# Kernel tuning notes

Hardware: AMD Instinct MI355X
Metric: run time of the kernel (lower is better)

The kernel has to match this reference:

```python
import jax, jax.numpy as jnp
import numpy as np

COMMITMENT_COST = 0.25
EMBEDDING_DIM = 64
NUM_EMBEDDINGS = 512
BATCH, SEQ = 64, 4096


def setup_inputs() -> dict:
    key = jax.random.key(0)
    k1, k2, k3 = jax.random.split(key, 3)
    return {
        "inputs": jax.random.normal(k1, (BATCH, SEQ, EMBEDDING_DIM), dtype=jnp.float32),
        "embedding": jax.random.normal(k2, (NUM_EMBEDDINGS, EMBEDDING_DIM), dtype=jnp.float32),
        "ema_cluster_size": jax.random.uniform(k3, (NUM_EMBEDDINGS,), dtype=jnp.float32),
    }


def reference(inputs, embedding, ema_cluster_size):
    # inputs: [B, T, D]; embedding: [K, D]; ema_cluster_size: [K]
    input_shape = inputs.shape
    flat = inputs.reshape(-1, EMBEDDING_DIM)  # [N, D]
    distances = (
        jnp.sum(flat * flat, axis=1, keepdims=True)
        + jnp.sum(embedding * embedding, axis=1)[None, :]
        - 2.0 * (flat @ embedding.T)
    )
    # cluster-size weighting (as in the source module)
    distances = distances * jnp.sqrt(ema_cluster_size)[None, :]
    encoding_indices = jnp.argmin(distances, axis=1)  # [N]
    # one-hot @ codebook == gather
    quantized = embedding[encoding_indices].reshape(input_shape)
    e_latent_loss = jnp.mean((jax.lax.stop_gradient(quantized) - inputs) ** 2)
    loss = COMMITMENT_COST * e_latent_loss
    # straight-through estimator
    quantized_st = inputs + jax.lax.stop_gradient(quantized - inputs)
    return quantized_st, loss, encoding_indices[:, None]
```

## Files before the change

### kernel.cpp

```cpp
#include <hip/hip_runtime.h>
#include <math.h>

#define D 64
#define K 512

typedef __attribute__((ext_vector_type(8))) short short8;
typedef __attribute__((ext_vector_type(4))) float f32x4;

#define WS_E2    256
#define WS_SQ    2304
#define WS_ETS   4352
#define WS_BP    8448
#define WS_WL    139520
#define WS_PART  1188096
#define WS_PART2 1204480

#define KEYMASK 0xFFFFFE00u
#define DIST_BIAS 0.0625f

__device__ __forceinline__ unsigned short f32_to_bf16_rne(float f)
{
    unsigned int u = __float_as_uint(f);
    unsigned int r = (u + 0x7FFFu + ((u >> 16) & 1u)) >> 16;
    return (unsigned short)r;
}
__device__ __forceinline__ float bf16_to_f32(unsigned short h)
{
    return __uint_as_float(((unsigned int)h) << 16);
}

__device__ __forceinline__ float np_sumsq64(const float* v)
{
#pragma clang fp contract(off)
    float p[64];
#pragma unroll
    for (int i = 0; i < 64; ++i) p[i] = v[i] * v[i];
    float r[8];
#pragma unroll
    for (int j = 0; j < 8; ++j) r[j] = p[j];
#pragma unroll
    for (int b = 8; b < 64; b += 8) {
#pragma unroll
        for (int j = 0; j < 8; ++j) r[j] += p[b + j];
    }
    return ((r[0] + r[1]) + (r[2] + r[3])) + ((r[4] + r[5]) + (r[6] + r[7]));
}

__global__ __launch_bounds__(256) void vq_pack_prep(
    const float* __restrict__ emb,
    const float* __restrict__ cs,
    unsigned short* __restrict__ Bp,
    float* __restrict__ e2,
    float* __restrict__ sq,
    float2* __restrict__ ets,
    int* __restrict__ cnt)
{
    int i = blockIdx.x * blockDim.x + threadIdx.x;
    if (i < 65536) {
        int j    = i & 7;
        int lane = (i >> 3) & 63;
        int frag = (i >> 9) & 3;
        int t    = (i >> 11) & 31;
        int kc   = frag & 1;
        int sB   = frag >> 1;
        int code = t * 16 + (lane & 15);
        int d    = kc * 32 + (lane >> 4) * 8 + j;
        float v = emb[code * 64 + d];
        unsigned short b0 = f32_to_bf16_rne(v);
        Bp[i] = (sB == 0) ? b0 : f32_to_bf16_rne(v - bf16_to_f32(b0));
    } else if (i < 66048) {
        int k = i - 65536;
        float er[64];
        const float* ek = emb + (size_t)k * D;
#pragma unroll
        for (int d = 0; d < 64; ++d) er[d] = ek[d];
        float e2v = np_sumsq64(er);
        float sqv = (float)sqrt((double)cs[k]);
        e2[k] = e2v;
        sq[k] = sqv;
        ets[k] = make_float2(e2v * sqv + DIST_BIAS, 2.0f * sqv);
    } else if (i == 66048) {
        *cnt = 0;
    }
}

__global__ __launch_bounds__(512) void vq_screen(
    const float* __restrict__ x,
    const float* __restrict__ emb,
    const float2* __restrict__ ets,
    const unsigned short* __restrict__ Bp,
    float* __restrict__ out_q,
    float* __restrict__ out_idx,
    int* __restrict__ wl,
    int* __restrict__ cnt,
    double* __restrict__ partial)
{
    __shared__ unsigned short BpS[65536];
    __shared__ double ls[8];

    const int wave = threadIdx.x >> 6;
    const int lane = threadIdx.x & 63;
    const int quad = lane >> 4;
    const int n16  = lane & 15;

    {
        const float4* src = (const float4*)Bp;
        float4* dst = (float4*)BpS;
#pragma unroll
        for (int it = 0; it < 16; ++it)
            dst[threadIdx.x + it * 512] = src[threadIdx.x + it * 512];
    }
    __syncthreads();

    double s = 0.0;

    for (int pass = 0; pass < 2; ++pass) {
        const int n0 = blockIdx.x * 1024 + pass * 512 + wave * 64;

        short8 A0[4][2], A1[4][2];
        f32x4 negx2h[4];
#pragma unroll
        for (int rt = 0; rt < 4; ++rt) {
            float sx = 0.0f;
#pragma unroll
            for (int kc = 0; kc < 2; ++kc) {
                const float* src = x + (size_t)(n0 + rt * 16 + n16) * 64
                                   + kc * 32 + quad * 8;
                float4 v0 = *(const float4*)(src);
                float4 v1 = *(const float4*)(src + 4);
                float xv[8] = {v0.x, v0.y, v0.z, v0.w, v1.x, v1.y, v1.z, v1.w};
#pragma unroll
                for (int j = 0; j < 8; ++j) {
                    float v = xv[j];
                    unsigned short b0 = f32_to_bf16_rne(v);
                    unsigned short b1 = f32_to_bf16_rne(v - bf16_to_f32(b0));
                    A0[rt][kc][j] = (short)b0;
                    A1[rt][kc][j] = (short)b1;
                    sx = fmaf(v, v, sx);
                }
            }
            sx += __shfl_xor(sx, 16, 64);
            sx += __shfl_xor(sx, 32, 64);
#pragma unroll
            for (int r = 0; r < 4; ++r)
                negx2h[rt][r] = -0.5f * __shfl(sx, quad * 4 + r, 64);
        }

        unsigned k1[4][4], k2[4][4];
#pragma unroll
        for (int rt = 0; rt < 4; ++rt)
#pragma unroll
            for (int r = 0; r < 4; ++r) { k1[rt][r] = 0xFFFFFFFFu; k2[rt][r] = 0xFFFFFFFFu; }

#pragma unroll 2
        for (int t = 0; t < 32; ++t) {
            const unsigned short* bp = BpS + t * 2048 + lane * 8;
            const short8 B00 = *(const short8*)(bp);
            const short8 B01 = *(const short8*)(bp + 512);
            const short8 B10 = *(const short8*)(bp + 1024);
            const short8 B11 = *(const short8*)(bp + 1536);
            float2 et = ets[t * 16 + n16];
            unsigned cbits = (unsigned)(t * 16 + n16);

#pragma unroll
            for (int rt = 0; rt < 4; ++rt) {
                f32x4 acc = negx2h[rt];
                acc = __builtin_amdgcn_mfma_f32_16x16x32_bf16(A0[rt][0], B00, acc, 0, 0, 0);
                acc = __builtin_amdgcn_mfma_f32_16x16x32_bf16(A0[rt][1], B01, acc, 0, 0, 0);
                acc = __builtin_amdgcn_mfma_f32_16x16x32_bf16(A0[rt][0], B10, acc, 0, 0, 0);
                acc = __builtin_amdgcn_mfma_f32_16x16x32_bf16(A0[rt][1], B11, acc, 0, 0, 0);
                acc = __builtin_amdgcn_mfma_f32_16x16x32_bf16(A1[rt][0], B00, acc, 0, 0, 0);
                acc = __builtin_amdgcn_mfma_f32_16x16x32_bf16(A1[rt][1], B01, acc, 0, 0, 0);

#pragma unroll
                for (int r = 0; r < 4; ++r) {
                    float dist = fmaf(-et.y, acc[r], et.x);
                    unsigned key = (__float_as_uint(dist) & KEYMASK) | cbits;
                    unsigned a1 = k1[rt][r];
                    unsigned a2;
                    asm("v_med3_u32 %0, %1, %2, %3"
                        : "=v"(a2) : "v"(a1), "v"(k2[rt][r]), "v"(key));
                    k2[rt][r] = a2;
                    k1[rt][r] = a1 < key ? a1 : key;
                }
            }
        }

#pragma unroll
        for (int rt = 0; rt < 4; ++rt)
#pragma unroll
            for (int r = 0; r < 4; ++r) {
                unsigned a1 = k1[rt][r], a2 = k2[rt][r];
#pragma unroll
                for (int w = 1; w < 16; w <<= 1) {
                    unsigned o1 = (unsigned)__shfl_xor((int)a1, w, 64);
                    unsigned o2 = (unsigned)__shfl_xor((int)a2, w, 64);
                    unsigned mx  = a1 > o1 ? a1 : o1;
                    a1 = a1 < o1 ? a1 : o1;
                    unsigned mn2 = a2 < o2 ? a2 : o2;
                    a2 = mn2 < mx ? mn2 : mx;
                }
                k1[rt][r] = a1; k2[rt][r] = a2;
            }

        unsigned pk[4][4];
#pragma unroll
        for (int rt = 0; rt < 4; ++rt)
#pragma unroll
            for (int r = 0; r < 4; ++r) {
                float d1f = __uint_as_float(k1[rt][r] & KEYMASK);
                float d2f = __uint_as_float(k2[rt][r] & KEYMASK);
                int   i1  = (int)(k1[rt][r] & 0x1FFu);
                int   flg = (d2f - d1f) <= (0.01f + 2.0e-4f * d2f);
                pk[rt][r] = (unsigned)i1 | (flg ? 0x8000u : 0u);
                if (n16 == 0) {
                    int p = n0 + rt * 16 + quad * 4 + r;
                    out_idx[p] = (float)i1;
                    if (flg) { int slot = atomicAdd(cnt, 1); wl[slot] = p; }
                }
            }

        int src = (n16 >> 2) * 16 + n16;
#pragma unroll
        for (int rt = 0; rt < 4; ++rt) {
            unsigned p0 = (unsigned)__shfl((int)pk[rt][0], src, 64);
            unsigned p1 = (unsigned)__shfl((int)pk[rt][1], src, 64);
            unsigned p2 = (unsigned)__shfl((int)pk[rt][2], src, 64);
            unsigned p3 = (unsigned)__shfl((int)pk[rt][3], src, 64);
            int rr = n16 & 3;
            unsigned pm = (rr == 0) ? p0 : (rr == 1) ? p1 : (rr == 2) ? p2 : p3;
            int bim = (int)(pm & 0x1FFu);
            int flg = (int)((pm >> 15) & 1u);
            if (!flg) {
                int prow = n0 + rt * 16 + n16;
#pragma unroll
                for (int kc = 0; kc < 2; ++kc) {
                    const float* xs = x   + (size_t)prow * 64 + kc * 32 + quad * 8;
                    const float* es = emb + (size_t)bim  * 64 + kc * 32 + quad * 8;
                    float4 xv0 = *(const float4*)(xs);
                    float4 xv1 = *(const float4*)(xs + 4);
                    float4 ev0 = *(const float4*)(es);
                    float4 ev1 = *(const float4*)(es + 4);
                    float4 o0, o1;
                    float t0, t1, t2, t3, t4, t5, t6, t7;
                    {
#pragma clang fp contract(off)
                        t0 = ev0.x - xv0.x; o0.x = xv0.x + t0;
                        t1 = ev0.y - xv0.y; o0.y = xv0.y + t1;
                        t2 = ev0.z - xv0.z; o0.z = xv0.z + t2;
                        t3 = ev0.w - xv0.w; o0.w = xv0.w + t3;
                        t4 = ev1.x - xv1.x; o1.x = xv1.x + t4;
                        t5 = ev1.y - xv1.y; o1.y = xv1.y + t5;
                        t6 = ev1.z - xv1.z; o1.z = xv1.z + t6;
                        t7 = ev1.w - xv1.w; o1.w = xv1.w + t7;
                    }
                    float* od = out_q + (size_t)prow * 64 + kc * 32 + quad * 8;
                    *(float4*)(od)     = o0;
                    *(float4*)(od + 4) = o1;
                    s += (double)t0 * t0 + (double)t1 * t1
                       + (double)t2 * t2 + (double)t3 * t3
                       + (double)t4 * t4 + (double)t5 * t5
                       + (double)t6 * t6 + (double)t7 * t7;
                }
            }
        }
    }

#pragma unroll
    for (int off = 32; off > 0; off >>= 1)
        s += __shfl_down(s, off, 64);
    if (lane == 0) ls[wave] = s;
    __syncthreads();
    if (threadIdx.x == 0)
        partial[blockIdx.x] = ls[0] + ls[1] + ls[2] + ls[3]
                            + ls[4] + ls[5] + ls[6] + ls[7];
}

__global__ __launch_bounds__(256) void vq_exact(
    const float* __restrict__ x,
    const float* __restrict__ emb,
    const float* __restrict__ e2,
    const float* __restrict__ sq,
    const int* __restrict__ wl,
    const int* __restrict__ cnt,
    float* __restrict__ out_idx,
    float* __restrict__ out_q,
    double* __restrict__ partial2)
{
    const int lane = threadIdx.x & 63;
    const int gw   = blockIdx.x * 4 + (threadIdx.x >> 6);
    const int nw   = gridDim.x * 4;
    const int cv   = *cnt;

    for (int w = gw; w < cv; w += nw) {
        int p = wl[w];
        const float* xrow = x + (size_t)p * 64;
        float row[64];
#pragma unroll
        for (int i = 0; i < 16; ++i) {
            float4 v = ((const float4*)xrow)[i];
            row[4 * i + 0] = v.x; row[4 * i + 1] = v.y;
            row[4 * i + 2] = v.z; row[4 * i + 3] = v.w;
        }
        float x2 = np_sumsq64(row);

        float bd = INFINITY;
        int   bc = 0;
        for (int t = 0; t < 8; ++t) {
            int c = t * 64 + lane;
            const float* er = emb + (size_t)c * 64;
            float acc = 0.0f;
#pragma unroll
            for (int d = 0; d < 64; ++d)
                acc = fmaf(row[d], er[d], acc);
            float dist;
            {
#pragma clang fp contract(off)
                dist = ((x2 + e2[c]) - 2.0f * acc) * sq[c];
            }
            if (dist < bd) { bd = dist; bc = c; }
        }
#pragma unroll
        for (int wd = 1; wd < 64; wd <<= 1) {
            float od = __shfl_xor(bd, wd, 64);
            int   oc = __shfl_xor(bc, wd, 64);
            if (od < bd || (od == bd && oc < bc)) { bd = od; bc = oc; }
        }
        if (lane == 0) out_idx[p] = (float)bc;

        float xv = x[(size_t)p * 64 + lane];
        float qv = emb[(size_t)bc * 64 + lane];
        float t, o;
        {
#pragma clang fp contract(off)
            t = qv - xv;
            o = xv + t;
        }
        out_q[(size_t)p * 64 + lane] = o;
        double dd = (double)t * (double)t;
#pragma unroll
        for (int off = 32; off > 0; off >>= 1)
            dd += __shfl_down(dd, off, 64);
        if (lane == 0) partial2[w] = dd;
    }
}

__global__ __launch_bounds__(256) void vq_finalize(
    const double* __restrict__ partial,
    const double* __restrict__ partial2,
    const int* __restrict__ cnt,
    float* __restrict__ loss_out,
    int nblk, double inv_count)
{
    double s = 0.0;
    for (int i = threadIdx.x; i < nblk; i += 256) s += partial[i];
    int cv = *cnt;
    for (int w = threadIdx.x; w < cv; w += 256) s += partial2[w];
#pragma unroll
    for (int off = 32; off > 0; off >>= 1)
        s += __shfl_down(s, off, 64);
    __shared__ double ls[4];
    if ((threadIdx.x & 63) == 0) ls[threadIdx.x >> 6] = s;
    __syncthreads();
    if (threadIdx.x == 0) {
        double total = ls[0] + ls[1] + ls[2] + ls[3];
        loss_out[0] = (float)(0.25 * total * inv_count);
    }
}

extern "C" void kernel_launch(void* const* d_in, const int* in_sizes, int n_in,
                              void* d_out, int out_size, void* d_ws, size_t ws_size,
                              hipStream_t stream)
{
    const float* x   = (const float*)d_in[0];
    const float* emb = (const float*)d_in[1];
    const float* cs  = (const float*)d_in[2];

    const int N = in_sizes[0] / D;

    float* out      = (float*)d_out;
    float* out_q    = out;
    float* out_loss = out + (size_t)N * D;
    float* out_idx  = out_loss + 1;

    char* ws = (char*)d_ws;
    int*            cnt      = (int*)ws;
    float*          e2       = (float*)(ws + WS_E2);
    float*          sq       = (float*)(ws + WS_SQ);
    float2*         ets      = (float2*)(ws + WS_ETS);
    unsigned short* Bp       = (unsigned short*)(ws + WS_BP);
    int*            wl       = (int*)(ws + WS_WL);
    double*         partial  = (double*)(ws + WS_PART);
    double*         partial2 = (double*)(ws + WS_PART2);

    const int nblk_screen = N / 1024;

    vq_pack_prep<<<259, 256, 0, stream>>>(emb, cs, Bp, e2, sq, ets, cnt);
    vq_screen<<<nblk_screen, 512, 0, stream>>>(x, emb, ets, Bp,
                                               out_q, out_idx, wl, cnt, partial);
    vq_exact<<<512, 256, 0, stream>>>(x, emb, e2, sq, wl, cnt,
                                      out_idx, out_q, partial2);
    vq_finalize<<<1, 256, 0, stream>>>(partial, partial2, cnt, out_loss,
                                       nblk_screen, 1.0 / ((double)N * (double)D));
}
```

Measured before the change: 204.3 us.

## Halve screen LDS footprint by staging codebook in two halves, one pass per block

The screening kernel now keeps only half of the packed bf16 codebook in shared memory (64KB instead of 128KB). It runs the first 256 codes, then reloads the second half between barriers. It also caches the ets table in LDS, and each block handles 512 rows in a single pass instead of 1024 rows in two, so twice as many blocks launch. The smaller LDS footprint is meant to let two blocks share a CU and to spread work over more blocks, at the cost of loading the codebook twice per block with an extra barrier in the middle.

```diff
diff --git a/kernel.cpp b/kernel.cpp
--- a/kernel.cpp
+++ b/kernel.cpp
@@ -95,173 +95,216 @@
     int* __restrict__ cnt,
     double* __restrict__ partial)
 {
-    __shared__ unsigned short BpS[65536];
+    __shared__ unsigned short BpS[32768];
+    __shared__ float2 etsS[512];
     __shared__ double ls[8];
 
     const int wave = threadIdx.x >> 6;
     const int lane = threadIdx.x & 63;
     const int quad = lane >> 4;
     const int n16  = lane & 15;
+    const int n0   = blockIdx.x * 512 + wave * 64;
 
     {
         const float4* src = (const float4*)Bp;
         float4* dst = (float4*)BpS;
 #pragma unroll
-        for (int it = 0; it < 16; ++it)
+        for (int it = 0; it < 8; ++it)
             dst[threadIdx.x + it * 512] = src[threadIdx.x + it * 512];
+        etsS[threadIdx.x] = ets[threadIdx.x];
     }
     __syncthreads();
 
     double s = 0.0;
 
-    for (int pass = 0; pass < 2; ++pass) {
-        const int n0 = blockIdx.x * 1024 + pass * 512 + wave * 64;
-
-        short8 A0[4][2], A1[4][2];
-        f32x4 negx2h[4];
+    short8 A0[4][2], A1[4][2];
+    f32x4 negx2h[4];
+#pragma unroll
+    for (int rt = 0; rt < 4; ++rt) {
+        float sx = 0.0f;
+#pragma unroll
+        for (int kc = 0; kc < 2; ++kc) {
+            const float* src = x + (size_t)(n0 + rt * 16 + n16) * 64
+                               + kc * 32 + quad * 8;
+            float4 v0 = *(const float4*)(src);
+            float4 v1 = *(const float4*)(src + 4);
+            float xv[8] = {v0.x, v0.y, v0.z, v0.w, v1.x, v1.y, v1.z, v1.w};
+#pragma unroll
+            for (int j = 0; j < 8; ++j) {
+                float v = xv[j];
+                unsigned short b0 = f32_to_bf16_rne(v);
+                unsigned short b1 = f32_to_bf16_rne(v - bf16_to_f32(b0));
+                A0[rt][kc][j] = (short)b0;
+                A1[rt][kc][j] = (short)b1;
+                sx = fmaf(v, v, sx);
+            }
+        }
+        sx += __shfl_xor(sx, 16, 64);
+        sx += __shfl_xor(sx, 32, 64);
+#pragma unroll
+        for (int r = 0; r < 4; ++r)
+            negx2h[rt][r] = -0.5f * __shfl(sx, quad * 4 + r, 64);
+    }
+
+    unsigned k1[4][4], k2[4][4];
+#pragma unroll
+    for (int rt = 0; rt < 4; ++rt)
+#pragma unroll
+        for (int r = 0; r < 4; ++r) { k1[rt][r] = 0xFFFFFFFFu; k2[rt][r] = 0xFFFFFFFFu; }
+
+#pragma unroll 2
+    for (int t = 0; t < 16; ++t) {
+        const unsigned short* bp = BpS + t * 2048 + lane * 8;
+        const short8 B00 = *(const short8*)(bp);
+        const short8 B01 = *(const short8*)(bp + 512);
+        const short8 B10 = *(const short8*)(bp + 1024);
+        const short8 B11 = *(const short8*)(bp + 1536);
+        float2 et = etsS[t * 16 + n16];
+        unsigned cbits = (unsigned)(t * 16 + n16);
+
 #pragma unroll
         for (int rt = 0; rt < 4; ++rt) {
-            float sx = 0.0f;
+            f32x4 acc = negx2h[rt];
+            acc = __builtin_amdgcn_mfma_f32_16x16x32_bf16(A0[rt][0], B00, acc, 0, 0, 0);
+            acc = __builtin_amdgcn_mfma_f32_16x16x32_bf16(A0[rt][1], B01, acc, 0, 0, 0);
+            acc = __builtin_amdgcn_mfma_f32_16x16x32_bf16(A0[rt][0], B10, acc, 0, 0, 0);
+            acc = __builtin_amdgcn_mfma_f32_16x16x32_bf16(A0[rt][1], B11, acc, 0, 0, 0);
+            acc = __builtin_amdgcn_mfma_f32_16x16x32_bf16(A1[rt][0], B00, acc, 0, 0, 0);
+            acc = __builtin_amdgcn_mfma_f32_16x16x32_bf16(A1[rt][1], B01, acc, 0, 0, 0);
+
+#pragma unroll
+            for (int r = 0; r < 4; ++r) {
+                float dist = fmaf(-et.y, acc[r], et.x);
+                unsigned key = (__float_as_uint(dist) & KEYMASK) | cbits;
+                unsigned a1 = k1[rt][r];
+                unsigned a2;
+                asm("v_med3_u32 %0, %1, %2, %3"
+                    : "=v"(a2) : "v"(a1), "v"(k2[rt][r]), "v"(key));
+                k2[rt][r] = a2;
+                k1[rt][r] = a1 < key ? a1 : key;
+            }
+        }
+    }
+
+    __syncthreads();
+    {
+        const float4* src = (const float4*)(Bp + 32768);
+        float4* dst = (float4*)BpS;
+#pragma unroll
+        for (int it = 0; it < 8; ++it)
+            dst[threadIdx.x + it * 512] = src[threadIdx.x + it * 512];
+    }
+    __syncthreads();
+
+#pragma unroll 2
+    for (int t = 16; t < 32; ++t) {
+        const unsigned short* bp = BpS + (t - 16) * 2048 + lane * 8;
+        const short8 B00 = *(const short8*)(bp);
+        const short8 B01 = *(const short8*)(bp + 512);
+        const short8 B10 = *(const short8*)(bp + 1024);
+        const short8 B11 = *(const short8*)(bp + 1536);
+        float2 et = etsS[t * 16 + n16];
+        unsigned cbits = (unsigned)(t * 16 + n16);
+
+#pragma unroll
+        for (int rt = 0; rt < 4; ++rt) {
+            f32x4 acc = negx2h[rt];
+            acc = __builtin_amdgcn_mfma_f32_16x16x32_bf16(A0[rt][0], B00, acc, 0, 0, 0);
+            acc = __builtin_amdgcn_mfma_f32_16x16x32_bf16(A0[rt][1], B01, acc, 0, 0, 0);
+            acc = __builtin_amdgcn_mfma_f32_16x16x32_bf16(A0[rt][0], B10, acc, 0, 0, 0);
+            acc = __builtin_amdgcn_mfma_f32_16x16x32_bf16(A0[rt][1], B11, acc, 0, 0, 0);
+            acc = __builtin_amdgcn_mfma_f32_16x16x32_bf16(A1[rt][0], B00, acc, 0, 0, 0);
+            acc = __builtin_amdgcn_mfma_f32_16x16x32_bf16(A1[rt][1], B01, acc, 0, 0, 0);
+
+#pragma unroll
+            for (int r = 0; r < 4; ++r) {
+                float dist = fmaf(-et.y, acc[r], et.x);
+                unsigned key = (__float_as_uint(dist) & KEYMASK) | cbits;
+                unsigned a1 = k1[rt][r];
+                unsigned a2;
+                asm("v_med3_u32 %0, %1, %2, %3"
+                    : "=v"(a2) : "v"(a1), "v"(k2[rt][r]), "v"(key));
+                k2[rt][r] = a2;
+                k1[rt][r] = a1 < key ? a1 : key;
+            }
+        }
+    }
+
+#pragma unroll
+    for (int rt = 0; rt < 4; ++rt)
+#pragma unroll
+        for (int r = 0; r < 4; ++r) {
+            unsigned a1 = k1[rt][r], a2 = k2[rt][r];
+#pragma unroll
+            for (int w = 1; w < 16; w <<= 1) {
+                unsigned o1 = (unsigned)__shfl_xor((int)a1, w, 64);
+                unsigned o2 = (unsigned)__shfl_xor((int)a2, w, 64);
+                unsigned mx  = a1 > o1 ? a1 : o1;
+                a1 = a1 < o1 ? a1 : o1;
+                unsigned mn2 = a2 < o2 ? a2 : o2;
+                a2 = mn2 < mx ? mn2 : mx;
+            }
+            k1[rt][r] = a1; k2[rt][r] = a2;
+        }
+
+    unsigned pk[4][4];
+#pragma unroll
+    for (int rt = 0; rt < 4; ++rt)
+#pragma unroll
+        for (int r = 0; r < 4; ++r) {
+            float d1f = __uint_as_float(k1[rt][r] & KEYMASK);
+            float d2f = __uint_as_float(k2[rt][r] & KEYMASK);
+            int   i1  = (int)(k1[rt][r] & 0x1FFu);
+            int   flg = (d2f - d1f) <= (0.01f + 2.0e-4f * d2f);
+            pk[rt][r] = (unsigned)i1 | (flg ? 0x8000u : 0u);
+            if (n16 == 0) {
+                int p = n0 + rt * 16 + quad * 4 + r;
+                out_idx[p] = (float)i1;
+                if (flg) { int slot = atomicAdd(cnt, 1); wl[slot] = p; }
+            }
+        }
+
+    int src = (n16 >> 2) * 16 + n16;
+#pragma unroll
+    for (int rt = 0; rt < 4; ++rt) {
+        unsigned p0 = (unsigned)__shfl((int)pk[rt][0], src, 64);
+        unsigned p1 = (unsigned)__shfl((int)pk[rt][1], src, 64);
+        unsigned p2 = (unsigned)__shfl((int)pk[rt][2], src, 64);
+        unsigned p3 = (unsigned)__shfl((int)pk[rt][3], src, 64);
+        int rr = n16 & 3;
+        unsigned pm = (rr == 0) ? p0 : (rr == 1) ? p1 : (rr == 2) ? p2 : p3;
+        int bim = (int)(pm & 0x1FFu);
+        int flg = (int)((pm >> 15) & 1u);
+        if (!flg) {
+            int prow = n0 + rt * 16 + n16;
 #pragma unroll
             for (int kc = 0; kc < 2; ++kc) {
-                const float* src = x + (size_t)(n0 + rt * 16 + n16) * 64
-                                   + kc * 32 + quad * 8;
-                float4 v0 = *(const float4*)(src);
-                float4 v1 = *(const float4*)(src + 4);
-                float xv[8] = {v0.x, v0.y, v0.z, v0.w, v1.x, v1.y, v1.z, v1.w};
-#pragma unroll
-                for (int j = 0; j < 8; ++j) {
-                    float v = xv[j];
-                    unsigned short b0 = f32_to_bf16_rne(v);
-                    unsigned short b1 = f32_to_bf16_rne(v - bf16_to_f32(b0));
-                    A0[rt][kc][j] = (short)b0;
-                    A1[rt][kc][j] = (short)b1;
-                    sx = fmaf(v, v, sx);
+                const float* xs = x   + (size_t)prow * 64 + kc * 32 + quad * 8;
+                const float* es = emb + (size_t)bim  * 64 + kc * 32 + quad * 8;
+                float4 xv0 = *(const float4*)(xs);
+                float4 xv1 = *(const float4*)(xs + 4);
+                float4 ev0 = *(const float4*)(es);
+                float4 ev1 = *(const float4*)(es + 4);
+                float4 o0, o1;
+                float t0, t1, t2, t3, t4, t5, t6, t7;
+                {
+#pragma clang fp contract(off)
+                    t0 = ev0.x - xv0.x; o0.x = xv0.x + t0;
+                    t1 = ev0.y - xv0.y; o0.y = xv0.y + t1;
+                    t2 = ev0.z - xv0.z; o0.z = xv0.z + t2;
+                    t3 = ev0.w - xv0.w; o0.w = xv0.w + t3;
+                    t4 = ev1.x - xv1.x; o1.x = xv1.x + t4;
+                    t5 = ev1.y - xv1.y; o1.y = xv1.y + t5;
+                    t6 = ev1.z - xv1.z; o1.z = xv1.z + t6;
+                    t7 = ev1.w - xv1.w; o1.w = xv1.w + t7;
                 }
-            }
-            sx += __shfl_xor(sx, 16, 64);
-            sx += __shfl_xor(sx, 32, 64);
-#pragma unroll
-            for (int r = 0; r < 4; ++r)
-                negx2h[rt][r] = -0.5f * __shfl(sx, quad * 4 + r, 64);
-        }
-
-        unsigned k1[4][4], k2[4][4];
-#pragma unroll
-        for (int rt = 0; rt < 4; ++rt)
-#pragma unroll
-            for (int r = 0; r < 4; ++r) { k1[rt][r] = 0xFFFFFFFFu; k2[rt][r] = 0xFFFFFFFFu; }
-
-#pragma unroll 2
-        for (int t = 0; t < 32; ++t) {
-            const unsigned short* bp = BpS + t * 2048 + lane * 8;
-            const short8 B00 = *(const short8*)(bp);
-            const short8 B01 = *(const short8*)(bp + 512);
-            const short8 B10 = *(const short8*)(bp + 1024);
-            const short8 B11 = *(const short8*)(bp + 1536);
-            float2 et = ets[t * 16 + n16];
-            unsigned cbits = (unsigned)(t * 16 + n16);
-
-#pragma unroll
-            for (int rt = 0; rt < 4; ++rt) {
-                f32x4 acc = negx2h[rt];
-                acc = __builtin_amdgcn_mfma_f32_16x16x32_bf16(A0[rt][0], B00, acc, 0, 0, 0);
-                acc = __builtin_amdgcn_mfma_f32_16x16x32_bf16(A0[rt][1], B01, acc, 0, 0, 0);
-                acc = __builtin_amdgcn_mfma_f32_16x16x32_bf16(A0[rt][0], B10, acc, 0, 0, 0);
-                acc = __builtin_amdgcn_mfma_f32_16x16x32_bf16(A0[rt][1], B11, acc, 0, 0, 0);
-                acc = __builtin_amdgcn_mfma_f32_16x16x32_bf16(A1[rt][0], B00, acc, 0, 0, 0);
-                acc = __builtin_amdgcn_mfma_f32_16x16x32_bf16(A1[rt][1], B01, acc, 0, 0, 0);
-
-#pragma unroll
-                for (int r = 0; r < 4; ++r) {
-                    float dist = fmaf(-et.y, acc[r], et.x);
-                    unsigned key = (__float_as_uint(dist) & KEYMASK) | cbits;
-                    unsigned a1 = k1[rt][r];
-                    unsigned a2;
-                    asm("v_med3_u32 %0, %1, %2, %3"
-                        : "=v"(a2) : "v"(a1), "v"(k2[rt][r]), "v"(key));
-                    k2[rt][r] = a2;
-                    k1[rt][r] = a1 < key ? a1 : key;
-                }
-            }
-        }
-
-#pragma unroll
-        for (int rt = 0; rt < 4; ++rt)
-#pragma unroll
-            for (int r = 0; r < 4; ++r) {
-                unsigned a1 = k1[rt][r], a2 = k2[rt][r];
-#pragma unroll
-                for (int w = 1; w < 16; w <<= 1) {
-                    unsigned o1 = (unsigned)__shfl_xor((int)a1, w, 64);
-                    unsigned o2 = (unsigned)__shfl_xor((int)a2, w, 64);
-                    unsigned mx  = a1 > o1 ? a1 : o1;
-                    a1 = a1 < o1 ? a1 : o1;
-                    unsigned mn2 = a2 < o2 ? a2 : o2;
-                    a2 = mn2 < mx ? mn2 : mx;
-                }
-                k1[rt][r] = a1; k2[rt][r] = a2;
-            }
-
-        unsigned pk[4][4];
-#pragma unroll
-        for (int rt = 0; rt < 4; ++rt)
-#pragma unroll
-            for (int r = 0; r < 4; ++r) {
-                float d1f = __uint_as_float(k1[rt][r] & KEYMASK);
-                float d2f = __uint_as_float(k2[rt][r] & KEYMASK);
-                int   i1  = (int)(k1[rt][r] & 0x1FFu);
-                int   flg = (d2f - d1f) <= (0.01f + 2.0e-4f * d2f);
-                pk[rt][r] = (unsigned)i1 | (flg ? 0x8000u : 0u);
-                if (n16 == 0) {
-                    int p = n0 + rt * 16 + quad * 4 + r;
-                    out_idx[p] = (float)i1;
-                    if (flg) { int slot = atomicAdd(cnt, 1); wl[slot] = p; }
-                }
-            }
-
-        int src = (n16 >> 2) * 16 + n16;
-#pragma unroll
-        for (int rt = 0; rt < 4; ++rt) {
-            unsigned p0 = (unsigned)__shfl((int)pk[rt][0], src, 64);
-            unsigned p1 = (unsigned)__shfl((int)pk[rt][1], src, 64);
-            unsigned p2 = (unsigned)__shfl((int)pk[rt][2], src, 64);
-            unsigned p3 = (unsigned)__shfl((int)pk[rt][3], src, 64);
-            int rr = n16 & 3;
-            unsigned pm = (rr == 0) ? p0 : (rr == 1) ? p1 : (rr == 2) ? p2 : p3;
-            int bim = (int)(pm & 0x1FFu);
-            int flg = (int)((pm >> 15) & 1u);
-            if (!flg) {
-                int prow = n0 + rt * 16 + n16;
-#pragma unroll
-                for (int kc = 0; kc < 2; ++kc) {
-                    const float* xs = x   + (size_t)prow * 64 + kc * 32 + quad * 8;
-                    const float* es = emb + (size_t)bim  * 64 + kc * 32 + quad * 8;
-                    float4 xv0 = *(const float4*)(xs);
-                    float4 xv1 = *(const float4*)(xs + 4);
-                    float4 ev0 = *(const float4*)(es);
-                    float4 ev1 = *(const float4*)(es + 4);
-                    float4 o0, o1;
-                    float t0, t1, t2, t3, t4, t5, t6, t7;
-                    {
-#pragma clang fp contract(off)
-                        t0 = ev0.x - xv0.x; o0.x = xv0.x + t0;
-                        t1 = ev0.y - xv0.y; o0.y = xv0.y + t1;
-                        t2 = ev0.z - xv0.z; o0.z = xv0.z + t2;
-                        t3 = ev0.w - xv0.w; o0.w = xv0.w + t3;
-                        t4 = ev1.x - xv1.x; o1.x = xv1.x + t4;
-                        t5 = ev1.y - xv1.y; o1.y = xv1.y + t5;
-                        t6 = ev1.z - xv1.z; o1.z = xv1.z + t6;
-                        t7 = ev1.w - xv1.w; o1.w = xv1.w + t7;
-                    }
-                    float* od = out_q + (size_t)prow * 64 + kc * 32 + quad * 8;
-                    *(float4*)(od)     = o0;
-                    *(float4*)(od + 4) = o1;
-                    s += (double)t0 * t0 + (double)t1 * t1
-                       + (double)t2 * t2 + (double)t3 * t3
-                       + (double)t4 * t4 + (double)t5 * t5
-                       + (double)t6 * t6 + (double)t7 * t7;
-                }
+                float* od = out_q + (size_t)prow * 64 + kc * 32 + quad * 8;
+                *(float4*)(od)     = o0;
+                *(float4*)(od + 4) = o1;
+                s += (double)t0 * t0 + (double)t1 * t1
+                   + (double)t2 * t2 + (double)t3 * t3
+                   + (double)t4 * t4 + (double)t5 * t5
+                   + (double)t6 * t6 + (double)t7 * t7;
             }
         }
     }
@@ -393,7 +436,7 @@
     double*         partial  = (double*)(ws + WS_PART);
     double*         partial2 = (double*)(ws + WS_PART2);
 
-    const int nblk_screen = N / 1024;
+    const int nblk_screen = N / 512;
 
     vq_pack_prep<<<259, 256, 0, stream>>>(emb, cs, Bp, e2, sq, ets, cnt);
     vq_screen<<<nblk_screen, 512, 0, stream>>>(x, emb, ets, Bp,
```

New measurement: 210.8 us. 1.03x slower.

## Fuse codebook packing and exact rescoring into the screening kernel

Applied to the files above, without the earlier changes.

Removes the separate pack/prep and exact-rescore kernels. Each screening block now builds the bf16 hi/lo codebook fragments and the per-code norm and scale tables directly in shared memory. It keeps a block-local worklist of ambiguous rows and rescores them in exact fp32 after the MFMA pass. This cuts two launches, the global worklist atomics and the partial2 traffic. The cost is that all 256 blocks redundantly recompute the codebook packing and norms, and shared memory use grows by about 12KB per block.

```diff
diff --git a/kernel.cpp b/kernel.cpp
--- a/kernel.cpp
+++ b/kernel.cpp
@@ -7,13 +7,7 @@
 typedef __attribute__((ext_vector_type(8))) short short8;
 typedef __attribute__((ext_vector_type(4))) float f32x4;
 
-#define WS_E2    256
-#define WS_SQ    2304
-#define WS_ETS   4352
-#define WS_BP    8448
-#define WS_WL    139520
 #define WS_PART  1188096
-#define WS_PART2 1204480
 
 #define KEYMASK 0xFFFFFE00u
 #define DIST_BIAS 0.0625f
@@ -46,56 +40,20 @@
     return ((r[0] + r[1]) + (r[2] + r[3])) + ((r[4] + r[5]) + (r[6] + r[7]));
 }
 
-__global__ __launch_bounds__(256) void vq_pack_prep(
-    const float* __restrict__ emb,
-    const float* __restrict__ cs,
-    unsigned short* __restrict__ Bp,
-    float* __restrict__ e2,
-    float* __restrict__ sq,
-    float2* __restrict__ ets,
-    int* __restrict__ cnt)
-{
-    int i = blockIdx.x * blockDim.x + threadIdx.x;
-    if (i < 65536) {
-        int j    = i & 7;
-        int lane = (i >> 3) & 63;
-        int frag = (i >> 9) & 3;
-        int t    = (i >> 11) & 31;
-        int kc   = frag & 1;
-        int sB   = frag >> 1;
-        int code = t * 16 + (lane & 15);
-        int d    = kc * 32 + (lane >> 4) * 8 + j;
-        float v = emb[code * 64 + d];
-        unsigned short b0 = f32_to_bf16_rne(v);
-        Bp[i] = (sB == 0) ? b0 : f32_to_bf16_rne(v - bf16_to_f32(b0));
-    } else if (i < 66048) {
-        int k = i - 65536;
-        float er[64];
-        const float* ek = emb + (size_t)k * D;
-#pragma unroll
-        for (int d = 0; d < 64; ++d) er[d] = ek[d];
-        float e2v = np_sumsq64(er);
-        float sqv = (float)sqrt((double)cs[k]);
-        e2[k] = e2v;
-        sq[k] = sqv;
-        ets[k] = make_float2(e2v * sqv + DIST_BIAS, 2.0f * sqv);
-    } else if (i == 66048) {
-        *cnt = 0;
-    }
-}
-
 __global__ __launch_bounds__(512) void vq_screen(
     const float* __restrict__ x,
     const float* __restrict__ emb,
-    const float2* __restrict__ ets,
-    const unsigned short* __restrict__ Bp,
+    const float* __restrict__ cs,
     float* __restrict__ out_q,
     float* __restrict__ out_idx,
-    int* __restrict__ wl,
-    int* __restrict__ cnt,
     double* __restrict__ partial)
 {
     __shared__ unsigned short BpS[65536];
+    __shared__ float2 etsS[512];
+    __shared__ float  e2S[512];
+    __shared__ float  sqS[512];
+    __shared__ int    lwl[1024];
+    __shared__ int    lcnt;
     __shared__ double ls[8];
 
     const int wave = threadIdx.x >> 6;
@@ -103,13 +61,34 @@
     const int quad = lane >> 4;
     const int n16  = lane & 15;
 
+    for (int it = 0; it < 64; ++it) {
+        int i2    = it * 512 + threadIdx.x;
+        int j     = i2 & 7;
+        int lane2 = (i2 >> 3) & 63;
+        int kc    = (i2 >> 9) & 1;
+        int t     = (i2 >> 10) & 31;
+        int code  = t * 16 + (lane2 & 15);
+        int d     = kc * 32 + (lane2 >> 4) * 8 + j;
+        float v = emb[code * 64 + d];
+        unsigned short b0 = f32_to_bf16_rne(v);
+        unsigned short b1 = f32_to_bf16_rne(v - bf16_to_f32(b0));
+        int e0 = t * 2048 + kc * 512 + (i2 & 511);
+        BpS[e0]        = b0;
+        BpS[e0 + 1024] = b1;
+    }
     {
-        const float4* src = (const float4*)Bp;
-        float4* dst = (float4*)BpS;
-#pragma unroll
-        for (int it = 0; it < 16; ++it)
-            dst[threadIdx.x + it * 512] = src[threadIdx.x + it * 512];
-    }
+        int k = threadIdx.x & 511;
+        float er[64];
+        const float* ek = emb + (size_t)k * D;
+#pragma unroll
+        for (int d = 0; d < 64; ++d) er[d] = ek[d];
+        float e2v = np_sumsq64(er);
+        float sqv = (float)sqrt((double)cs[k]);
+        etsS[k] = make_float2(e2v * sqv + DIST_BIAS, 2.0f * sqv);
+        e2S[k]  = e2v;
+        sqS[k]  = sqv;
+    }
+    if (threadIdx.x == 0) lcnt = 0;
     __syncthreads();
 
     double s = 0.0;
@@ -159,7 +138,7 @@
             const short8 B01 = *(const short8*)(bp + 512);
             const short8 B10 = *(const short8*)(bp + 1024);
             const short8 B11 = *(const short8*)(bp + 1536);
-            float2 et = ets[t * 16 + n16];
+            float2 et = etsS[t * 16 + n16];
             unsigned cbits = (unsigned)(t * 16 + n16);
 
 #pragma unroll
@@ -216,7 +195,7 @@
                 if (n16 == 0) {
                     int p = n0 + rt * 16 + quad * 4 + r;
                     out_idx[p] = (float)i1;
-                    if (flg) { int slot = atomicAdd(cnt, 1); wl[slot] = p; }
+                    if (flg) { int slot = atomicAdd(&lcnt, 1); lwl[slot] = p; }
                 }
             }
 
@@ -266,6 +245,62 @@
         }
     }
 
+    __syncthreads();
+    {
+        const int nf = lcnt;
+        for (int w = wave; w < nf; w += 8) {
+            int p = lwl[w];
+            const float* xrow = x + (size_t)p * 64;
+            float row[64];
+#pragma unroll
+            for (int i = 0; i < 16; ++i) {
+                float4 v = ((const float4*)xrow)[i];
+                row[4 * i + 0] = v.x; row[4 * i + 1] = v.y;
+                row[4 * i + 2] = v.z; row[4 * i + 3] = v.w;
+            }
+            float x2 = np_sumsq64(row);
+
+            float bd = INFINITY;
+            int   bc = 0;
+            for (int t = 0; t < 8; ++t) {
+                int c = t * 64 + lane;
+                const float* er = emb + (size_t)c * 64;
+                float acc = 0.0f;
+#pragma unroll
+                for (int d = 0; d < 64; ++d)
+                    acc = fmaf(row[d], er[d], acc);
+                float dist;
+                {
+#pragma clang fp contract(off)
+                    dist = ((x2 + e2S[c]) - 2.0f * acc) * sqS[c];
+                }
+                if (dist < bd) { bd = dist; bc = c; }
+            }
+#pragma unroll
+            for (int wd = 1; wd < 64; wd <<= 1) {
+                float od = __shfl_xor(bd, wd, 64);
+                int   oc = __shfl_xor(bc, wd, 64);
+                if (od < bd || (od == bd && oc < bc)) { bd = od; bc = oc; }
+            }
+            if (lane == 0) out_idx[p] = (float)bc;
+
+            float xv = x[(size_t)p * 64 + lane];
+            float qv = emb[(size_t)bc * 64 + lane];
+            float t, o;
+            {
+#pragma clang fp contract(off)
+                t = qv - xv;
+                o = xv + t;
+            }
+            out_q[(size_t)p * 64 + lane] = o;
+            double dd = (double)t * (double)t;
+#pragma unroll
+            for (int off = 32; off > 0; off >>= 1)
+                dd += __shfl_down(dd, off, 64);
+            if (lane == 0) s += dd;
+        }
+    }
+
 #pragma unroll
     for (int off = 32; off > 0; off >>= 1)
         s += __shfl_down(s, off, 64);
@@ -276,86 +311,13 @@
                             + ls[4] + ls[5] + ls[6] + ls[7];
 }
 
-__global__ __launch_bounds__(256) void vq_exact(
-    const float* __restrict__ x,
-    const float* __restrict__ emb,
-    const float* __restrict__ e2,
-    const float* __restrict__ sq,
-    const int* __restrict__ wl,
-    const int* __restrict__ cnt,
-    float* __restrict__ out_idx,
-    float* __restrict__ out_q,
-    double* __restrict__ partial2)
-{
-    const int lane = threadIdx.x & 63;
-    const int gw   = blockIdx.x * 4 + (threadIdx.x >> 6);
-    const int nw   = gridDim.x * 4;
-    const int cv   = *cnt;
-
-    for (int w = gw; w < cv; w += nw) {
-        int p = wl[w];
-        const float* xrow = x + (size_t)p * 64;
-        float row[64];
-#pragma unroll
-        for (int i = 0; i < 16; ++i) {
-            float4 v = ((const float4*)xrow)[i];
-            row[4 * i + 0] = v.x; row[4 * i + 1] = v.y;
-            row[4 * i + 2] = v.z; row[4 * i + 3] = v.w;
-        }
-        float x2 = np_sumsq64(row);
-
-        float bd = INFINITY;
-        int   bc = 0;
-        for (int t = 0; t < 8; ++t) {
-            int c = t * 64 + lane;
-            const float* er = emb + (size_t)c * 64;
-            float acc = 0.0f;
-#pragma unroll
-            for (int d = 0; d < 64; ++d)
-                acc = fmaf(row[d], er[d], acc);
-            float dist;
-            {
-#pragma clang fp contract(off)
-                dist = ((x2 + e2[c]) - 2.0f * acc) * sq[c];
-            }
-            if (dist < bd) { bd = dist; bc = c; }
-        }
-#pragma unroll
-        for (int wd = 1; wd < 64; wd <<= 1) {
-            float od = __shfl_xor(bd, wd, 64);
-            int   oc = __shfl_xor(bc, wd, 64);
-            if (od < bd || (od == bd && oc < bc)) { bd = od; bc = oc; }
-        }
-        if (lane == 0) out_idx[p] = (float)bc;
-
-        float xv = x[(size_t)p * 64 + lane];
-        float qv = emb[(size_t)bc * 64 + lane];
-        float t, o;
-        {
-#pragma clang fp contract(off)
-            t = qv - xv;
-            o = xv + t;
-        }
-        out_q[(size_t)p * 64 + lane] = o;
-        double dd = (double)t * (double)t;
-#pragma unroll
-        for (int off = 32; off > 0; off >>= 1)
-            dd += __shfl_down(dd, off, 64);
-        if (lane == 0) partial2[w] = dd;
-    }
-}
-
 __global__ __launch_bounds__(256) void vq_finalize(
     const double* __restrict__ partial,
-    const double* __restrict__ partial2,
-    const int* __restrict__ cnt,
     float* __restrict__ loss_out,
     int nblk, double inv_count)
 {
     double s = 0.0;
     for (int i = threadIdx.x; i < nblk; i += 256) s += partial[i];
-    int cv = *cnt;
-    for (int w = threadIdx.x; w < cv; w += 256) s += partial2[w];
 #pragma unroll
     for (int off = 32; off > 0; off >>= 1)
         s += __shfl_down(s, off, 64);
@@ -384,22 +346,12 @@
     float* out_idx  = out_loss + 1;
 
     char* ws = (char*)d_ws;
-    int*            cnt      = (int*)ws;
-    float*          e2       = (float*)(ws + WS_E2);
-    float*          sq       = (float*)(ws + WS_SQ);
-    float2*         ets      = (float2*)(ws + WS_ETS);
-    unsigned short* Bp       = (unsigned short*)(ws + WS_BP);
-    int*            wl       = (int*)(ws + WS_WL);
-    double*         partial  = (double*)(ws + WS_PART);
-    double*         partial2 = (double*)(ws + WS_PART2);
+    double* partial = (double*)(ws + WS_PART);
 
     const int nblk_screen = N / 1024;
 
-    vq_pack_prep<<<259, 256, 0, stream>>>(emb, cs, Bp, e2, sq, ets, cnt);
-    vq_screen<<<nblk_screen, 512, 0, stream>>>(x, emb, ets, Bp,
-                                               out_q, out_idx, wl, cnt, partial);
-    vq_exact<<<512, 256, 0, stream>>>(x, emb, e2, sq, wl, cnt,
-                                      out_idx, out_q, partial2);
-    vq_finalize<<<1, 256, 0, stream>>>(partial, partial2, cnt, out_loss,
-                                       nblk_screen, 1.0 / ((double)N * (double)D));
-}
+    vq_screen<<<nblk_screen, 512, 0, stream>>>(x, emb, cs,
+                                               out_q, out_idx, partial);
+    vq_finalize<<<1, 256, 0, stream>>>(partial, out_loss, nblk_screen,
+                                       1.0 / ((double)N * (double)D));
+}
```

New measurement: 210.0 us. +2.8%, slower.

## Fuse exact rescoring of flagged rows into screen kernel with block-local worklist

Applied to the files above, without the earlier changes.

Drops the separate vq_exact kernel. Each screen block now collects its ambiguous rows in a shared-memory worklist with a shared atomic counter, then rescores them in exact fp32 at the end of the same kernel, adding the result to the block's loss partial. The ets, e2 and sq tables are also staged into LDS. This removes one launch, the global atomic counter and the worklist round trip through global memory. The cost is that flagged-row work becomes tail work inside each block, which can be unevenly spread across blocks, plus about 10 KB of extra LDS on top of the existing 128 KB.

```diff
diff --git a/kernel.cpp b/kernel.cpp
--- a/kernel.cpp
+++ b/kernel.cpp
@@ -11,9 +11,7 @@
 #define WS_SQ    2304
 #define WS_ETS   4352
 #define WS_BP    8448
-#define WS_WL    139520
 #define WS_PART  1188096
-#define WS_PART2 1204480
 
 #define KEYMASK 0xFFFFFE00u
 #define DIST_BIAS 0.0625f
@@ -87,15 +85,20 @@
 __global__ __launch_bounds__(512) void vq_screen(
     const float* __restrict__ x,
     const float* __restrict__ emb,
+    const float* __restrict__ e2,
+    const float* __restrict__ sq,
     const float2* __restrict__ ets,
     const unsigned short* __restrict__ Bp,
     float* __restrict__ out_q,
     float* __restrict__ out_idx,
-    int* __restrict__ wl,
-    int* __restrict__ cnt,
     double* __restrict__ partial)
 {
     __shared__ unsigned short BpS[65536];
+    __shared__ float2 etsS[512];
+    __shared__ float  e2S[512];
+    __shared__ float  sqS[512];
+    __shared__ int    lwl[1024];
+    __shared__ int    lcnt;
     __shared__ double ls[8];
 
     const int wave = threadIdx.x >> 6;
@@ -109,7 +112,11 @@
 #pragma unroll
         for (int it = 0; it < 16; ++it)
             dst[threadIdx.x + it * 512] = src[threadIdx.x + it * 512];
-    }
+        etsS[threadIdx.x] = ets[threadIdx.x];
+        e2S[threadIdx.x]  = e2[threadIdx.x];
+        sqS[threadIdx.x]  = sq[threadIdx.x];
+    }
+    if (threadIdx.x == 0) lcnt = 0;
     __syncthreads();
 
     double s = 0.0;
@@ -159,7 +166,7 @@
             const short8 B01 = *(const short8*)(bp + 512);
             const short8 B10 = *(const short8*)(bp + 1024);
             const short8 B11 = *(const short8*)(bp + 1536);
-            float2 et = ets[t * 16 + n16];
+            float2 et = etsS[t * 16 + n16];
             unsigned cbits = (unsigned)(t * 16 + n16);
 
 #pragma unroll
@@ -216,7 +223,7 @@
                 if (n16 == 0) {
                     int p = n0 + rt * 16 + quad * 4 + r;
                     out_idx[p] = (float)i1;
-                    if (flg) { int slot = atomicAdd(cnt, 1); wl[slot] = p; }
+                    if (flg) { int slot = atomicAdd(&lcnt, 1); lwl[slot] = p; }
                 }
             }
 
@@ -266,6 +273,62 @@
         }
     }
 
+    __syncthreads();
+    {
+        const int nf = lcnt;
+        for (int w = wave; w < nf; w += 8) {
+            int p = lwl[w];
+            const float* xrow = x + (size_t)p * 64;
+            float row[64];
+#pragma unroll
+            for (int i = 0; i < 16; ++i) {
+                float4 v = ((const float4*)xrow)[i];
+                row[4 * i + 0] = v.x; row[4 * i + 1] = v.y;
+                row[4 * i + 2] = v.z; row[4 * i + 3] = v.w;
+            }
+            float x2 = np_sumsq64(row);
+
+            float bd = INFINITY;
+            int   bc = 0;
+            for (int t = 0; t < 8; ++t) {
+                int c = t * 64 + lane;
+                const float* er = emb + (size_t)c * 64;
+                float acc = 0.0f;
+#pragma unroll
+                for (int d = 0; d < 64; ++d)
+                    acc = fmaf(row[d], er[d], acc);
+                float dist;
+                {
+#pragma clang fp contract(off)
+                    dist = ((x2 + e2S[c]) - 2.0f * acc) * sqS[c];
+                }
+                if (dist < bd) { bd = dist; bc = c; }
+            }
+#pragma unroll
+            for (int wd = 1; wd < 64; wd <<= 1) {
+                float od = __shfl_xor(bd, wd, 64);
+                int   oc = __shfl_xor(bc, wd, 64);
+                if (od < bd || (od == bd && oc < bc)) { bd = od; bc = oc; }
+            }
+            if (lane == 0) out_idx[p] = (float)bc;
+
+            float xv = x[(size_t)p * 64 + lane];
+            float qv = emb[(size_t)bc * 64 + lane];
+            float t, o;
+            {
+#pragma clang fp contract(off)
+                t = qv - xv;
+                o = xv + t;
+            }
+            out_q[(size_t)p * 64 + lane] = o;
+            double dd = (double)t * (double)t;
+#pragma unroll
+            for (int off = 32; off > 0; off >>= 1)
+                dd += __shfl_down(dd, off, 64);
+            if (lane == 0) s += dd;
+        }
+    }
+
 #pragma unroll
     for (int off = 32; off > 0; off >>= 1)
         s += __shfl_down(s, off, 64);
@@ -276,86 +339,13 @@
                             + ls[4] + ls[5] + ls[6] + ls[7];
 }
 
-__global__ __launch_bounds__(256) void vq_exact(
-    const float* __restrict__ x,
-    const float* __restrict__ emb,
-    const float* __restrict__ e2,
-    const float* __restrict__ sq,
-    const int* __restrict__ wl,
-    const int* __restrict__ cnt,
-    float* __restrict__ out_idx,
-    float* __restrict__ out_q,
-    double* __restrict__ partial2)
-{
-    const int lane = threadIdx.x & 63;
-    const int gw   = blockIdx.x * 4 + (threadIdx.x >> 6);
-    const int nw   = gridDim.x * 4;
-    const int cv   = *cnt;
-
-    for (int w = gw; w < cv; w += nw) {
-        int p = wl[w];
-        const float* xrow = x + (size_t)p * 64;
-        float row[64];
-#pragma unroll
-        for (int i = 0; i < 16; ++i) {
-            float4 v = ((const float4*)xrow)[i];
-            row[4 * i + 0] = v.x; row[4 * i + 1] = v.y;
-            row[4 * i + 2] = v.z; row[4 * i + 3] = v.w;
-        }
-        float x2 = np_sumsq64(row);
-
-        float bd = INFINITY;
-        int   bc = 0;
-        for (int t = 0; t < 8; ++t) {
-            int c = t * 64 + lane;
-            const float* er = emb + (size_t)c * 64;
-            float acc = 0.0f;
-#pragma unroll
-            for (int d = 0; d < 64; ++d)
-                acc = fmaf(row[d], er[d], acc);
-            float dist;
-            {
-#pragma clang fp contract(off)
-                dist = ((x2 + e2[c]) - 2.0f * acc) * sq[c];
-            }
-            if (dist < bd) { bd = dist; bc = c; }
-        }
-#pragma unroll
-        for (int wd = 1; wd < 64; wd <<= 1) {
-            float od = __shfl_xor(bd, wd, 64);
-            int   oc = __shfl_xor(bc, wd, 64);
-            if (od < bd || (od == bd && oc < bc)) { bd = od; bc = oc; }
-        }
-        if (lane == 0) out_idx[p] = (float)bc;
-
-        float xv = x[(size_t)p * 64 + lane];
-        float qv = emb[(size_t)bc * 64 + lane];
-        float t, o;
-        {
-#pragma clang fp contract(off)
-            t = qv - xv;
-            o = xv + t;
-        }
-        out_q[(size_t)p * 64 + lane] = o;
-        double dd = (double)t * (double)t;
-#pragma unroll
-        for (int off = 32; off > 0; off >>= 1)
-            dd += __shfl_down(dd, off, 64);
-        if (lane == 0) partial2[w] = dd;
-    }
-}
-
 __global__ __launch_bounds__(256) void vq_finalize(
     const double* __restrict__ partial,
-    const double* __restrict__ partial2,
-    const int* __restrict__ cnt,
     float* __restrict__ loss_out,
     int nblk, double inv_count)
 {
     double s = 0.0;
     for (int i = threadIdx.x; i < nblk; i += 256) s += partial[i];
-    int cv = *cnt;
-    for (int w = threadIdx.x; w < cv; w += 256) s += partial2[w];
 #pragma unroll
     for (int off = 32; off > 0; off >>= 1)
         s += __shfl_down(s, off, 64);
@@ -384,22 +374,18 @@
     float* out_idx  = out_loss + 1;
 
     char* ws = (char*)d_ws;
-    int*            cnt      = (int*)ws;
-    float*          e2       = (float*)(ws + WS_E2);
-    float*          sq       = (float*)(ws + WS_SQ);
-    float2*         ets      = (float2*)(ws + WS_ETS);
-    unsigned short* Bp       = (unsigned short*)(ws + WS_BP);
-    int*            wl       = (int*)(ws + WS_WL);
-    double*         partial  = (double*)(ws + WS_PART);
-    double*         partial2 = (double*)(ws + WS_PART2);
+    int*            cnt     = (int*)ws;
+    float*          e2      = (float*)(ws + WS_E2);
+    float*          sq      = (float*)(ws + WS_SQ);
+    float2*         ets     = (float2*)(ws + WS_ETS);
+    unsigned short* Bp      = (unsigned short*)(ws + WS_BP);
+    double*         partial = (double*)(ws + WS_PART);
 
     const int nblk_screen = N / 1024;
 
     vq_pack_prep<<<259, 256, 0, stream>>>(emb, cs, Bp, e2, sq, ets, cnt);
-    vq_screen<<<nblk_screen, 512, 0, stream>>>(x, emb, ets, Bp,
-                                               out_q, out_idx, wl, cnt, partial);
-    vq_exact<<<512, 256, 0, stream>>>(x, emb, e2, sq, wl, cnt,
-                                      out_idx, out_q, partial2);
-    vq_finalize<<<1, 256, 0, stream>>>(partial, partial2, cnt, out_loss,
-                                       nblk_screen, 1.0 / ((double)N * (double)D));
-}
+    vq_screen<<<nblk_screen, 512, 0, stream>>>(x, emb, e2, sq, ets, Bp,
+                                               out_q, out_idx, partial);
+    vq_finalize<<<1, 256, 0, stream>>>(partial, out_loss, nblk_screen,
+                                       1.0 / ((double)N * (double)D));
+}
```

After: 208.6 us. +2.1%, slower.
